# Kernel tuning notes

Measured on AMD Instinct MI355X. Metric: run time of the kernel, lower is better.

Reference implementation:

```python
import jax, jax.numpy as jnp
import numpy as np

D_MODEL = 512
NUM_HEADS = 8
DEPTH = D_MODEL // NUM_HEADS
BATCH = 16
SEQ = 1024


def setup_inputs() -> dict:
    key = jax.random.key(0)
    kq, kk, kv, k1, k2, k3, k4 = jax.random.split(key, 7)
    scale = 1.0 / np.sqrt(D_MODEL)
    return {
        "v": jax.random.normal(kv, (BATCH, SEQ, D_MODEL), jnp.float32),
        "k": jax.random.normal(kk, (BATCH, SEQ, D_MODEL), jnp.float32),
        "q": jax.random.normal(kq, (BATCH, SEQ, D_MODEL), jnp.float32),
        "mask": jnp.ones((BATCH, SEQ), jnp.float32),
        # Conv1D(kernel_size=1, use_bias=False) == per-token Linear: x @ W, W [d_in, d_out]
        "Wq": jax.random.normal(k1, (D_MODEL, D_MODEL), jnp.float32) * scale,
        "Wk": jax.random.normal(k2, (D_MODEL, D_MODEL), jnp.float32) * scale,
        "Wv": jax.random.normal(k3, (D_MODEL, D_MODEL), jnp.float32) * scale,
        "Wo": jax.random.normal(k4, (D_MODEL, D_MODEL), jnp.float32) * scale,
    }


def _split_heads(x, batch):
    # [b, s, d_model] -> [b, h, s, depth]
    return x.reshape(batch, -1, NUM_HEADS, DEPTH).transpose(0, 2, 1, 3)


def reference(v, k, q, mask, Wq, Wk, Wv, Wo):
    batch = q.shape[0]
    qh = _split_heads(q @ Wq, batch)  # [b,h,sq,dh]
    kh = _split_heads(k @ Wk, batch)  # [b,h,sk,dh]
    vh = _split_heads(v @ Wv, batch)  # [b,h,sk,dh]

    dk = jnp.asarray(DEPTH, qh.dtype)
    logits = jnp.einsum("bhqd,bhkd->bhqk", qh, kh) / jnp.sqrt(dk)
    # additive padding mask, broadcast [b,1,1,sk]
    logits = logits + (1.0 - mask[:, None, None, :]) * (-1e9)
    attention_weights = jax.nn.softmax(logits, axis=-1)  # [b,h,sq,sk]

    ctx = jnp.einsum("bhqk,bhkd->bhqd", attention_weights, vh)
    ctx = ctx.transpose(0, 2, 1, 3).reshape(batch, -1, D_MODEL)
    output = ctx @ Wo
    return output, attention_weights
```

## Files before the change

kernel.cpp:

```cpp
#include <hip/hip_runtime.h>


typedef _Float16 f16;
typedef _Float16 f16x8 __attribute__((ext_vector_type(8)));
typedef _Float16 f16x4 __attribute__((ext_vector_type(4)));
typedef float f32x4 __attribute__((ext_vector_type(4)));

#define DEVINL __device__ __forceinline__

static constexpr int BATCH = 16, SEQ = 1024, DM = 512, NH = 8, DH = 64;

DEVINL void async16(void* lds, const void* g) {
  __builtin_amdgcn_global_load_lds(
      (const __attribute__((address_space(1))) unsigned int*)g,
      (__attribute__((address_space(3))) unsigned int*)lds, 16, 0, 0);
}

__global__ __launch_bounds__(256) void prep_wt_k(
    const float* __restrict__ Wq, const float* __restrict__ Wk,
    const float* __restrict__ Wv, const float* __restrict__ Wo,
    f16* __restrict__ WT) {
  __shared__ float t[32][33];
  const int w = blockIdx.z;
  const float* src = (w == 0) ? Wq : (w == 1) ? Wk : (w == 2) ? Wv : Wo;
  const int k0 = blockIdx.y * 32, n0 = blockIdx.x * 32;
  const int r0 = threadIdx.x >> 5, c = threadIdx.x & 31;
#pragma unroll
  for (int i = 0; i < 4; ++i)
    t[i * 8 + r0][c] = src[(size_t)(k0 + i * 8 + r0) * DM + n0 + c];
  __syncthreads();
  f16* dst = WT + (size_t)w * DM * DM;
#pragma unroll
  for (int i = 0; i < 4; ++i)
    dst[(size_t)(n0 + i * 8 + r0) * DM + k0 + c] = (f16)t[c][i * 8 + r0];
}

template <int MODE>
DEVINL void gemm_body(const float* __restrict__ A32, const f16* __restrict__ A16,
                      const f16* __restrict__ WTn, f16* __restrict__ O16,
                      float* __restrict__ O32, int m0, int n0, bool vt) {
  __shared__ __align__(16) f16 As[2][128 * 32];
  __shared__ __align__(16) f16 Bs[2][128 * 32];
  const int tid = threadIdx.x;
  const int lane = tid & 63, wave = tid >> 6;
  const int wr = wave >> 1, wc = wave & 1;
  const int lrow = lane & 15, lkg = lane >> 4;
  f32x4 acc[4][4] = {};

  f32x4 ar[4];

  auto stageB = [&](int kt, int buf) {
#pragma unroll
    for (int it = 0; it < 2; ++it) {
      const int o = (it * 256 + tid) * 16;
      const int n = o >> 6, kb = o & 63;
      async16((char*)&Bs[buf][0] + (it * 256 + wave * 64) * 16,
              (const char*)WTn + ((size_t)(n0 + n) * DM + kt * 32) * 2 + kb);
    }
  };
  auto stageA_async = [&](int kt, int buf) {
#pragma unroll
    for (int it = 0; it < 2; ++it) {
      const int o = (it * 256 + tid) * 16;
      const int row = o >> 6, kb = o & 63;
      async16((char*)&As[buf][0] + (it * 256 + wave * 64) * 16,
              (const char*)A16 + ((size_t)(m0 + row) * DM + kt * 32) * 2 + kb);
    }
  };
  auto loadA = [&](int kt) {
#pragma unroll
    for (int c = 0; c < 4; ++c) {
      const int idx = c * 256 + tid;
      const int row = idx >> 3, sub = idx & 7;
      ar[c] = *(const f32x4*)(A32 + (size_t)(m0 + row) * DM + kt * 32 + sub * 4);
    }
  };
  auto writeA = [&](int buf) {
#pragma unroll
    for (int c = 0; c < 4; ++c) {
      const int idx = c * 256 + tid;
      const int row = idx >> 3, sub = idx & 7;
      f16x4 t;
      t[0] = (f16)ar[c][0]; t[1] = (f16)ar[c][1];
      t[2] = (f16)ar[c][2]; t[3] = (f16)ar[c][3];
      *(f16x4*)&As[buf][row * 32 + sub * 4] = t;
    }
  };

  stageB(0, 0);
  if (MODE == 0) {
    loadA(0);
    writeA(0);
  } else {
    stageA_async(0, 0);
  }
  __syncthreads();

  for (int kt = 0; kt < DM / 32; ++kt) {
    const int cur = kt & 1;
    if (kt < DM / 32 - 1) {
      stageB(kt + 1, cur ^ 1);
      if (MODE == 0) loadA(kt + 1);
      else stageA_async(kt + 1, cur ^ 1);
    }
    f16x8 af[4], bf[4];
#pragma unroll
    for (int i = 0; i < 4; ++i)
      af[i] = *(const f16x8*)&As[cur][(wr * 64 + i * 16 + lrow) * 32 + lkg * 8];
#pragma unroll
    for (int j = 0; j < 4; ++j)
      bf[j] = *(const f16x8*)&Bs[cur][(wc * 64 + j * 16 + lrow) * 32 + lkg * 8];
#pragma unroll
    for (int i = 0; i < 4; ++i)
#pragma unroll
      for (int j = 0; j < 4; ++j)
        acc[i][j] = __builtin_amdgcn_mfma_f32_16x16x32_f16(af[i], bf[j], acc[i][j], 0, 0, 0);
    if (MODE == 0 && kt < DM / 32 - 1) writeA(cur ^ 1);
    __syncthreads();
  }

#pragma unroll
  for (int i = 0; i < 4; ++i) {
#pragma unroll
    for (int j = 0; j < 4; ++j) {
#pragma unroll
      for (int r = 0; r < 4; ++r) {
        const int m = m0 + wr * 64 + i * 16 + lkg * 4 + r;
        const int g = n0 + wc * 64 + j * 16 + lrow;
        if (MODE == 0) {
          const int b = m >> 10, s = m & 1023, hh = g >> 6, d = g & 63;
          if (vt)
            O16[(((size_t)b * NH + hh) * DH + d) * SEQ + s] = (f16)acc[i][j][r];
          else
            O16[(((size_t)b * NH + hh) * SEQ + s) * DH + d] = (f16)acc[i][j][r];
        } else {
          O32[(size_t)m * DM + g] = acc[i][j][r];
        }
      }
    }
  }
}

__global__ __launch_bounds__(256, 2) void proj_k(
    const float* __restrict__ q, const float* __restrict__ k, const float* __restrict__ v,
    const f16* __restrict__ WT, f16* __restrict__ Qh, f16* __restrict__ Kh,
    f16* __restrict__ Vh) {
  const int bid = blockIdx.x;
  const int wid = (bid & 7) * 192 + (bid >> 3);
  const int n_blk = wid & 3, m_blk = (wid >> 2) & 127, z = wid >> 9;
  const float* A = (z == 0) ? q : (z == 1) ? k : v;
  const f16* W = WT + (size_t)z * DM * DM;
  f16* O = (z == 0) ? Qh : (z == 1) ? Kh : Vh;
  gemm_body<0>(A, nullptr, W, O, nullptr, m_blk * 128, n_blk * 128, z == 2);
}

__global__ __launch_bounds__(256, 2) void outp_k(const f16* __restrict__ ctx,
                                                 const f16* __restrict__ WoT,
                                                 float* __restrict__ out0) {
  const int bid = blockIdx.x;
  const int wid = (bid & 7) * 64 + (bid >> 3);
  const int n_blk = wid & 3, m_blk = wid >> 2;
  gemm_body<1>(nullptr, ctx, WoT, nullptr, out0, m_blk * 128, n_blk * 128, false);
}

__global__ __launch_bounds__(256, 3) void attn_k(
    const f16* __restrict__ Qh, const f16* __restrict__ Kh, const f16* __restrict__ VTh,
    const float* __restrict__ mask, float* __restrict__ attnW, f16* __restrict__ ctx) {
  __shared__ __align__(16) f16 Ks[2][64 * 64];
  __shared__ __align__(16) f16 Vt[2][64 * 64];
  __shared__ __align__(16) f16 Ps[4][16 * 64];
  __shared__ __align__(16) float Ms[SEQ];
  const int tid = threadIdx.x;
  const int lane = tid & 63, wave = tid >> 6;
  const int lq = lane & 15, g = lane >> 4;
  const int bid = blockIdx.x;
  const int wid = (bid & 7) * 256 + (bid >> 3);
  const int qt = wid & 15, h = (wid >> 4) & 7, b = wid >> 7;
  const size_t bh = (size_t)b * NH + h;
  const char* Kbase = (const char*)(Kh + bh * SEQ * DH);
  const char* VTbase = (const char*)(VTh + bh * (size_t)DH * SEQ);
  const int q0 = qt * 64 + wave * 16;

  auto stageK = [&](int kt, int buf) {
    const char* KtileB = Kbase + (size_t)kt * 64 * DH * 2;
#pragma unroll
    for (int it = 0; it < 2; ++it) {
      const int o = (it * 256 + tid) * 16;
      const int key = o >> 7, slot = (o >> 4) & 7;
      async16((char*)&Ks[buf][0] + (it * 256 + wave * 64) * 16,
              KtileB + key * 128 + ((slot ^ (key & 7)) << 4));
    }
  };
  auto stageV = [&](int kt, int buf) {
    const char* VtileB = VTbase + (size_t)kt * 64 * 2;
#pragma unroll
    for (int it = 0; it < 2; ++it) {
      const int o = (it * 256 + tid) * 16;
      const int d = o >> 7, slot = (o >> 4) & 7;
      async16((char*)&Vt[buf][0] + (it * 256 + wave * 64) * 16,
              VtileB + (size_t)d * (SEQ * 2) + ((slot ^ (d & 7)) << 4));
    }
  };

  {
    f32x4 mv = *(const f32x4*)(mask + (size_t)b * SEQ + tid * 4);
    f32x4 bv;
    bv[0] = (1.0f - mv[0]) * (-1e9f);
    bv[1] = (1.0f - mv[1]) * (-1e9f);
    bv[2] = (1.0f - mv[2]) * (-1e9f);
    bv[3] = (1.0f - mv[3]) * (-1e9f);
    *(f32x4*)&Ms[tid * 4] = bv;
  }

  f16x8 aQ0, aQ1;
  {
    const f16* qp = Qh + (bh * SEQ + q0 + lq) * DH + g * 8;
    aQ0 = *(const f16x8*)qp;
    aQ1 = *(const f16x8*)(qp + 32);
  }

  stageK(0, 0);
  __syncthreads();
  float ssum = 0.0f;
  for (int kt = 0; kt < 16; ++kt) {
    const int cur = kt & 1;
    if (kt < 15) stageK(kt + 1, cur ^ 1);
    f32x4 lg[4] = {};
#pragma unroll
    for (int j = 0; j < 4; ++j) {
      const int krow = j * 16 + lq;
      f16x8 a0 = *(const f16x8*)((const char*)&Ks[cur][0] + krow * 128 + ((g ^ (krow & 7)) << 4));
      f16x8 a1 = *(const f16x8*)((const char*)&Ks[cur][0] + krow * 128 + (((4 + g) ^ (krow & 7)) << 4));
      lg[j] = __builtin_amdgcn_mfma_f32_16x16x32_f16(a0, aQ0, lg[j], 0, 0, 0);
      lg[j] = __builtin_amdgcn_mfma_f32_16x16x32_f16(a1, aQ1, lg[j], 0, 0, 0);
    }
#pragma unroll
    for (int j = 0; j < 4; ++j) {
      f32x4 bias = *(const f32x4*)&Ms[kt * 64 + j * 16 + g * 4];
#pragma unroll
      for (int r = 0; r < 4; ++r) ssum += __expf(lg[j][r] * 0.125f + bias[r]);
    }
    __syncthreads();
  }

  ssum += __shfl_xor(ssum, 16);
  ssum += __shfl_xor(ssum, 32);
  const float inv = 1.0f / ssum;

  f32x4 ctxacc[4] = {};
  float* awBase = attnW + (bh * SEQ + q0) * SEQ;

  stageK(0, 0);
  stageV(0, 0);
  __syncthreads();
  for (int kt = 0; kt < 16; ++kt) {
    const int cur = kt & 1;
    if (kt < 15) {
      stageK(kt + 1, cur ^ 1);
      stageV(kt + 1, cur ^ 1);
    }
    f32x4 lg[4] = {};
#pragma unroll
    for (int j = 0; j < 4; ++j) {
      const int krow = j * 16 + lq;
      f16x8 a0 = *(const f16x8*)((const char*)&Ks[cur][0] + krow * 128 + ((g ^ (krow & 7)) << 4));
      f16x8 a1 = *(const f16x8*)((const char*)&Ks[cur][0] + krow * 128 + (((4 + g) ^ (krow & 7)) << 4));
      lg[j] = __builtin_amdgcn_mfma_f32_16x16x32_f16(a0, aQ0, lg[j], 0, 0, 0);
      lg[j] = __builtin_amdgcn_mfma_f32_16x16x32_f16(a1, aQ1, lg[j], 0, 0, 0);
    }
#pragma unroll
    for (int j = 0; j < 4; ++j) {
      f32x4 bias = *(const f32x4*)&Ms[kt * 64 + j * 16 + g * 4];
      f32x4 w;
#pragma unroll
      for (int r = 0; r < 4; ++r) w[r] = __expf(lg[j][r] * 0.125f + bias[r]) * inv;
      *(f32x4*)(awBase + (size_t)lq * SEQ + kt * 64 + j * 16 + g * 4) = w;
      f16x4 pw;
      pw[0] = (f16)w[0]; pw[1] = (f16)w[1]; pw[2] = (f16)w[2]; pw[3] = (f16)w[3];
      const int slot = 2 * j + (g >> 1);
      *(f16x4*)((char*)&Ps[wave][0] + lq * 128 + ((slot ^ (lq & 7)) << 4) + 8 * (g & 1)) = pw;
    }
#pragma unroll
    for (int kk = 0; kk < 2; ++kk) {
      f16x8 aP = *(const f16x8*)((const char*)&Ps[wave][0] + lq * 128 +
                                 (((4 * kk + g) ^ (lq & 7)) << 4));
#pragma unroll
      for (int j2 = 0; j2 < 4; ++j2) {
        const int drow = j2 * 16 + lq;
        f16x8 bV = *(const f16x8*)((const char*)&Vt[cur][0] + drow * 128 +
                                   (((4 * kk + g) ^ (drow & 7)) << 4));
        ctxacc[j2] = __builtin_amdgcn_mfma_f32_16x16x32_f16(aP, bV, ctxacc[j2], 0, 0, 0);
      }
    }
    __syncthreads();
  }

#pragma unroll
  for (int j2 = 0; j2 < 4; ++j2)
#pragma unroll
    for (int r = 0; r < 4; ++r) {
      const int s = q0 + g * 4 + r;
      const int d = j2 * 16 + lq;
      ctx[(((size_t)b * SEQ + s) * NH + h) * DH + d] = (f16)ctxacc[j2][r];
    }
}

extern "C" void kernel_launch(void* const* d_in, const int* in_sizes, int n_in,
                              void* d_out, int out_size, void* d_ws, size_t ws_size,
                              hipStream_t stream) {
  const float* v = (const float*)d_in[0];
  const float* k = (const float*)d_in[1];
  const float* q = (const float*)d_in[2];
  const float* mask = (const float*)d_in[3];
  const float* Wq = (const float*)d_in[4];
  const float* Wk = (const float*)d_in[5];
  const float* Wv = (const float*)d_in[6];
  const float* Wo = (const float*)d_in[7];

  float* out0 = (float*)d_out;
  float* attnW = out0 + (size_t)BATCH * SEQ * DM;

  char* ws = (char*)d_ws;
  f16* WT = (f16*)ws;
  f16* Qh = (f16*)(ws + (size_t)4 * DM * DM * 2);
  f16* Kh = Qh + (size_t)BATCH * NH * SEQ * DH;
  f16* VTh = Kh + (size_t)BATCH * NH * SEQ * DH;
  f16* ctx = VTh + (size_t)BATCH * NH * SEQ * DH;

  prep_wt_k<<<dim3(16, 16, 4), 256, 0, stream>>>(Wq, Wk, Wv, Wo, WT);
  proj_k<<<dim3(1536), 256, 0, stream>>>(q, k, v, WT, Qh, Kh, VTh);
  attn_k<<<dim3(2048), 256, 0, stream>>>(Qh, Kh, VTh, mask, attnW, ctx);
  outp_k<<<dim3(512), 256, 0, stream>>>(ctx, WT + (size_t)3 * DM * DM, out0);
}
```

Measured before the change: 341.9 us.

## Cache unnormalized probabilities in LDS to skip recomputing QK^T in second pass

The first pass now writes fp16 exp(logits) for the wave's full 16x1024 row block into a large LDS buffer. The second pass reads them back instead of restaging K and redoing the QK^T MFMAs and exponentials. The softmax normalization is applied when writing attention weights, and once to the context accumulator at the end. This removes the duplicate K loads and score computation. In exchange, LDS use grows to roughly 150KB per block, which limits occupancy to one block per CU, and the stored attention weights now come from fp16-rounded exponentials.

```diff
diff --git a/kernel.cpp b/kernel.cpp
--- a/kernel.cpp
+++ b/kernel.cpp
@@ -163,12 +163,11 @@
   gemm_body<1>(nullptr, ctx, WoT, nullptr, out0, m_blk * 128, n_blk * 128, false);
 }
 
-__global__ __launch_bounds__(256, 3) void attn_k(
+__global__ __launch_bounds__(256, 1) void attn_k(
     const f16* __restrict__ Qh, const f16* __restrict__ Kh, const f16* __restrict__ VTh,
     const float* __restrict__ mask, float* __restrict__ attnW, f16* __restrict__ ctx) {
-  __shared__ __align__(16) f16 Ks[2][64 * 64];
-  __shared__ __align__(16) f16 Vt[2][64 * 64];
-  __shared__ __align__(16) f16 Ps[4][16 * 64];
+  __shared__ __align__(16) f16 st[2][64 * 64];
+  __shared__ __align__(16) f16 Pw[4][16 * 1024];
   __shared__ __align__(16) float Ms[SEQ];
   const int tid = threadIdx.x;
   const int lane = tid & 63, wave = tid >> 6;
@@ -187,7 +186,7 @@
     for (int it = 0; it < 2; ++it) {
       const int o = (it * 256 + tid) * 16;
       const int key = o >> 7, slot = (o >> 4) & 7;
-      async16((char*)&Ks[buf][0] + (it * 256 + wave * 64) * 16,
+      async16((char*)&st[buf][0] + (it * 256 + wave * 64) * 16,
               KtileB + key * 128 + ((slot ^ (key & 7)) << 4));
     }
   };
@@ -197,7 +196,7 @@
     for (int it = 0; it < 2; ++it) {
       const int o = (it * 256 + tid) * 16;
       const int d = o >> 7, slot = (o >> 4) & 7;
-      async16((char*)&Vt[buf][0] + (it * 256 + wave * 64) * 16,
+      async16((char*)&st[buf][0] + (it * 256 + wave * 64) * 16,
               VtileB + (size_t)d * (SEQ * 2) + ((slot ^ (d & 7)) << 4));
     }
   };
@@ -229,16 +228,23 @@
 #pragma unroll
     for (int j = 0; j < 4; ++j) {
       const int krow = j * 16 + lq;
-      f16x8 a0 = *(const f16x8*)((const char*)&Ks[cur][0] + krow * 128 + ((g ^ (krow & 7)) << 4));
-      f16x8 a1 = *(const f16x8*)((const char*)&Ks[cur][0] + krow * 128 + (((4 + g) ^ (krow & 7)) << 4));
+      f16x8 a0 = *(const f16x8*)((const char*)&st[cur][0] + krow * 128 + ((g ^ (krow & 7)) << 4));
+      f16x8 a1 = *(const f16x8*)((const char*)&st[cur][0] + krow * 128 + (((4 + g) ^ (krow & 7)) << 4));
       lg[j] = __builtin_amdgcn_mfma_f32_16x16x32_f16(a0, aQ0, lg[j], 0, 0, 0);
       lg[j] = __builtin_amdgcn_mfma_f32_16x16x32_f16(a1, aQ1, lg[j], 0, 0, 0);
     }
 #pragma unroll
     for (int j = 0; j < 4; ++j) {
       f32x4 bias = *(const f32x4*)&Ms[kt * 64 + j * 16 + g * 4];
-#pragma unroll
-      for (int r = 0; r < 4; ++r) ssum += __expf(lg[j][r] * 0.125f + bias[r]);
+      f16x4 pw;
+#pragma unroll
+      for (int r = 0; r < 4; ++r) {
+        const float p = __expf(lg[j][r] * 0.125f + bias[r]);
+        pw[r] = (f16)p;
+        ssum += (float)pw[r];
+      }
+      const int s = kt * 8 + j * 2 + (g >> 1);
+      *(f16x4*)((char*)&Pw[wave][0] + lq * 2048 + ((s ^ (lq & 7)) << 4) + (g & 1) * 8) = pw;
     }
     __syncthreads();
   }
@@ -250,44 +256,29 @@
   f32x4 ctxacc[4] = {};
   float* awBase = attnW + (bh * SEQ + q0) * SEQ;
 
-  stageK(0, 0);
   stageV(0, 0);
   __syncthreads();
   for (int kt = 0; kt < 16; ++kt) {
     const int cur = kt & 1;
-    if (kt < 15) {
-      stageK(kt + 1, cur ^ 1);
-      stageV(kt + 1, cur ^ 1);
-    }
-    f32x4 lg[4] = {};
+    if (kt < 15) stageV(kt + 1, cur ^ 1);
 #pragma unroll
     for (int j = 0; j < 4; ++j) {
-      const int krow = j * 16 + lq;
-      f16x8 a0 = *(const f16x8*)((const char*)&Ks[cur][0] + krow * 128 + ((g ^ (krow & 7)) << 4));
-      f16x8 a1 = *(const f16x8*)((const char*)&Ks[cur][0] + krow * 128 + (((4 + g) ^ (krow & 7)) << 4));
-      lg[j] = __builtin_amdgcn_mfma_f32_16x16x32_f16(a0, aQ0, lg[j], 0, 0, 0);
-      lg[j] = __builtin_amdgcn_mfma_f32_16x16x32_f16(a1, aQ1, lg[j], 0, 0, 0);
-    }
-#pragma unroll
-    for (int j = 0; j < 4; ++j) {
-      f32x4 bias = *(const f32x4*)&Ms[kt * 64 + j * 16 + g * 4];
+      const int s = kt * 8 + j * 2 + (g >> 1);
+      f16x4 pw = *(const f16x4*)((const char*)&Pw[wave][0] + lq * 2048 +
+                                 ((s ^ (lq & 7)) << 4) + (g & 1) * 8);
       f32x4 w;
-#pragma unroll
-      for (int r = 0; r < 4; ++r) w[r] = __expf(lg[j][r] * 0.125f + bias[r]) * inv;
+      w[0] = (float)pw[0] * inv; w[1] = (float)pw[1] * inv;
+      w[2] = (float)pw[2] * inv; w[3] = (float)pw[3] * inv;
       *(f32x4*)(awBase + (size_t)lq * SEQ + kt * 64 + j * 16 + g * 4) = w;
-      f16x4 pw;
-      pw[0] = (f16)w[0]; pw[1] = (f16)w[1]; pw[2] = (f16)w[2]; pw[3] = (f16)w[3];
-      const int slot = 2 * j + (g >> 1);
-      *(f16x4*)((char*)&Ps[wave][0] + lq * 128 + ((slot ^ (lq & 7)) << 4) + 8 * (g & 1)) = pw;
     }
 #pragma unroll
     for (int kk = 0; kk < 2; ++kk) {
-      f16x8 aP = *(const f16x8*)((const char*)&Ps[wave][0] + lq * 128 +
-                                 (((4 * kk + g) ^ (lq & 7)) << 4));
+      const int s = kt * 8 + kk * 4 + g;
+      f16x8 aP = *(const f16x8*)((const char*)&Pw[wave][0] + lq * 2048 + ((s ^ (lq & 7)) << 4));
 #pragma unroll
       for (int j2 = 0; j2 < 4; ++j2) {
         const int drow = j2 * 16 + lq;
-        f16x8 bV = *(const f16x8*)((const char*)&Vt[cur][0] + drow * 128 +
+        f16x8 bV = *(const f16x8*)((const char*)&st[cur][0] + drow * 128 +
                                    (((4 * kk + g) ^ (drow & 7)) << 4));
         ctxacc[j2] = __builtin_amdgcn_mfma_f32_16x16x32_f16(aP, bV, ctxacc[j2], 0, 0, 0);
       }
@@ -295,13 +286,17 @@
     __syncthreads();
   }
 
+  float invR[4];
+#pragma unroll
+  for (int r = 0; r < 4; ++r) invR[r] = __shfl(inv, g * 4 + r, 64);
+
 #pragma unroll
   for (int j2 = 0; j2 < 4; ++j2)
 #pragma unroll
     for (int r = 0; r < 4; ++r) {
       const int s = q0 + g * 4 + r;
       const int d = j2 * 16 + lq;
-      ctx[(((size_t)b * SEQ + s) * NH + h) * DH + d] = (f16)ctxacc[j2][r];
+      ctx[(((size_t)b * SEQ + s) * NH + h) * DH + d] = (f16)(ctxacc[j2][r] * invR[r]);
     }
 }
 
```

New measurement: 457.4 us. 33.8% more time.

## Process four query subtiles per attention block to reuse staged K/V tiles

Applied to the files above, without the earlier changes.

Each attention block now handles 256 queries (four 16-row subtiles per wave) instead of 64, so every K and V tile staged in LDS feeds four times as many MFMAs. The grid shrinks from 2048 to 512 blocks and the launch bound drops to 2 waves-per-EU to make room for the larger accumulator and register footprint. This is meant to cut redundant global K/V reads and LDS staging. The cost is higher register pressure, a larger Ps buffer in LDS, and fewer blocks to hide latency on the attention-weight stores.

```diff
diff --git a/kernel.cpp b/kernel.cpp
--- a/kernel.cpp
+++ b/kernel.cpp
@@ -163,23 +163,23 @@
   gemm_body<1>(nullptr, ctx, WoT, nullptr, out0, m_blk * 128, n_blk * 128, false);
 }
 
-__global__ __launch_bounds__(256, 3) void attn_k(
+__global__ __launch_bounds__(256, 2) void attn_k(
     const f16* __restrict__ Qh, const f16* __restrict__ Kh, const f16* __restrict__ VTh,
     const float* __restrict__ mask, float* __restrict__ attnW, f16* __restrict__ ctx) {
   __shared__ __align__(16) f16 Ks[2][64 * 64];
   __shared__ __align__(16) f16 Vt[2][64 * 64];
-  __shared__ __align__(16) f16 Ps[4][16 * 64];
+  __shared__ __align__(16) f16 Ps[4][4][16 * 64];
   __shared__ __align__(16) float Ms[SEQ];
   const int tid = threadIdx.x;
   const int lane = tid & 63, wave = tid >> 6;
   const int lq = lane & 15, g = lane >> 4;
   const int bid = blockIdx.x;
-  const int wid = (bid & 7) * 256 + (bid >> 3);
-  const int qt = wid & 15, h = (wid >> 4) & 7, b = wid >> 7;
+  const int wid = (bid & 7) * 64 + (bid >> 3);
+  const int qt4 = wid & 3, h = (wid >> 2) & 7, b = wid >> 5;
   const size_t bh = (size_t)b * NH + h;
   const char* Kbase = (const char*)(Kh + bh * SEQ * DH);
   const char* VTbase = (const char*)(VTh + bh * (size_t)DH * SEQ);
-  const int q0 = qt * 64 + wave * 16;
+  const int qbase = qt4 * 256 + wave * 16;
 
   auto stageK = [&](int kt, int buf) {
     const char* KtileB = Kbase + (size_t)kt * 64 * DH * 2;
@@ -212,43 +212,55 @@
     *(f32x4*)&Ms[tid * 4] = bv;
   }
 
-  f16x8 aQ0, aQ1;
-  {
-    const f16* qp = Qh + (bh * SEQ + q0 + lq) * DH + g * 8;
-    aQ0 = *(const f16x8*)qp;
-    aQ1 = *(const f16x8*)(qp + 32);
-  }
-
+  f16x8 aQ0[4], aQ1[4];
+#pragma unroll
+  for (int st = 0; st < 4; ++st) {
+    const f16* qp = Qh + (bh * SEQ + qbase + st * 64 + lq) * DH + g * 8;
+    aQ0[st] = *(const f16x8*)qp;
+    aQ1[st] = *(const f16x8*)(qp + 32);
+  }
+
+  float ssum[4] = {0.f, 0.f, 0.f, 0.f};
   stageK(0, 0);
   __syncthreads();
-  float ssum = 0.0f;
   for (int kt = 0; kt < 16; ++kt) {
     const int cur = kt & 1;
     if (kt < 15) stageK(kt + 1, cur ^ 1);
-    f32x4 lg[4] = {};
+    f16x8 a0[4], a1[4];
 #pragma unroll
     for (int j = 0; j < 4; ++j) {
       const int krow = j * 16 + lq;
-      f16x8 a0 = *(const f16x8*)((const char*)&Ks[cur][0] + krow * 128 + ((g ^ (krow & 7)) << 4));
-      f16x8 a1 = *(const f16x8*)((const char*)&Ks[cur][0] + krow * 128 + (((4 + g) ^ (krow & 7)) << 4));
-      lg[j] = __builtin_amdgcn_mfma_f32_16x16x32_f16(a0, aQ0, lg[j], 0, 0, 0);
-      lg[j] = __builtin_amdgcn_mfma_f32_16x16x32_f16(a1, aQ1, lg[j], 0, 0, 0);
-    }
-#pragma unroll
-    for (int j = 0; j < 4; ++j) {
-      f32x4 bias = *(const f32x4*)&Ms[kt * 64 + j * 16 + g * 4];
-#pragma unroll
-      for (int r = 0; r < 4; ++r) ssum += __expf(lg[j][r] * 0.125f + bias[r]);
+      a0[j] = *(const f16x8*)((const char*)&Ks[cur][0] + krow * 128 + ((g ^ (krow & 7)) << 4));
+      a1[j] = *(const f16x8*)((const char*)&Ks[cur][0] + krow * 128 + (((4 + g) ^ (krow & 7)) << 4));
+    }
+#pragma unroll
+    for (int st = 0; st < 4; ++st) {
+      f32x4 lg[4] = {};
+#pragma unroll
+      for (int j = 0; j < 4; ++j) {
+        lg[j] = __builtin_amdgcn_mfma_f32_16x16x32_f16(a0[j], aQ0[st], lg[j], 0, 0, 0);
+        lg[j] = __builtin_amdgcn_mfma_f32_16x16x32_f16(a1[j], aQ1[st], lg[j], 0, 0, 0);
+      }
+#pragma unroll
+      for (int j = 0; j < 4; ++j) {
+        f32x4 bias = *(const f32x4*)&Ms[kt * 64 + j * 16 + g * 4];
+#pragma unroll
+        for (int r = 0; r < 4; ++r) ssum[st] += __expf(lg[j][r] * 0.125f + bias[r]);
+      }
     }
     __syncthreads();
   }
 
-  ssum += __shfl_xor(ssum, 16);
-  ssum += __shfl_xor(ssum, 32);
-  const float inv = 1.0f / ssum;
-
-  f32x4 ctxacc[4] = {};
-  float* awBase = attnW + (bh * SEQ + q0) * SEQ;
+  float inv[4];
+#pragma unroll
+  for (int st = 0; st < 4; ++st) {
+    float s = ssum[st];
+    s += __shfl_xor(s, 16);
+    s += __shfl_xor(s, 32);
+    inv[st] = 1.0f / s;
+  }
+
+  f32x4 ctxacc[4][4] = {};
 
   stageK(0, 0);
   stageV(0, 0);
@@ -259,50 +271,68 @@
       stageK(kt + 1, cur ^ 1);
       stageV(kt + 1, cur ^ 1);
     }
-    f32x4 lg[4] = {};
+    f16x8 a0[4], a1[4];
 #pragma unroll
     for (int j = 0; j < 4; ++j) {
       const int krow = j * 16 + lq;
-      f16x8 a0 = *(const f16x8*)((const char*)&Ks[cur][0] + krow * 128 + ((g ^ (krow & 7)) << 4));
-      f16x8 a1 = *(const f16x8*)((const char*)&Ks[cur][0] + krow * 128 + (((4 + g) ^ (krow & 7)) << 4));
-      lg[j] = __builtin_amdgcn_mfma_f32_16x16x32_f16(a0, aQ0, lg[j], 0, 0, 0);
-      lg[j] = __builtin_amdgcn_mfma_f32_16x16x32_f16(a1, aQ1, lg[j], 0, 0, 0);
-    }
-#pragma unroll
-    for (int j = 0; j < 4; ++j) {
-      f32x4 bias = *(const f32x4*)&Ms[kt * 64 + j * 16 + g * 4];
-      f32x4 w;
-#pragma unroll
-      for (int r = 0; r < 4; ++r) w[r] = __expf(lg[j][r] * 0.125f + bias[r]) * inv;
-      *(f32x4*)(awBase + (size_t)lq * SEQ + kt * 64 + j * 16 + g * 4) = w;
-      f16x4 pw;
-      pw[0] = (f16)w[0]; pw[1] = (f16)w[1]; pw[2] = (f16)w[2]; pw[3] = (f16)w[3];
-      const int slot = 2 * j + (g >> 1);
-      *(f16x4*)((char*)&Ps[wave][0] + lq * 128 + ((slot ^ (lq & 7)) << 4) + 8 * (g & 1)) = pw;
+      a0[j] = *(const f16x8*)((const char*)&Ks[cur][0] + krow * 128 + ((g ^ (krow & 7)) << 4));
+      a1[j] = *(const f16x8*)((const char*)&Ks[cur][0] + krow * 128 + (((4 + g) ^ (krow & 7)) << 4));
+    }
+#pragma unroll
+    for (int st = 0; st < 4; ++st) {
+      f32x4 lg[4] = {};
+#pragma unroll
+      for (int j = 0; j < 4; ++j) {
+        lg[j] = __builtin_amdgcn_mfma_f32_16x16x32_f16(a0[j], aQ0[st], lg[j], 0, 0, 0);
+        lg[j] = __builtin_amdgcn_mfma_f32_16x16x32_f16(a1[j], aQ1[st], lg[j], 0, 0, 0);
+      }
+      float* awRow = attnW + ((bh * SEQ + qbase + st * 64 + lq) * SEQ) + kt * 64 + g * 4;
+      char* psBase = (char*)&Ps[wave][st][0] + lq * 128;
+#pragma unroll
+      for (int j = 0; j < 4; ++j) {
+        f32x4 bias = *(const f32x4*)&Ms[kt * 64 + j * 16 + g * 4];
+        f32x4 w;
+#pragma unroll
+        for (int r = 0; r < 4; ++r) w[r] = __expf(lg[j][r] * 0.125f + bias[r]) * inv[st];
+        *(f32x4*)(awRow + j * 16) = w;
+        f16x4 pw;
+        pw[0] = (f16)w[0]; pw[1] = (f16)w[1]; pw[2] = (f16)w[2]; pw[3] = (f16)w[3];
+        const int slot = 2 * j + (g >> 1);
+        *(f16x4*)(psBase + ((slot ^ (lq & 7)) << 4) + (g & 1) * 8) = pw;
+      }
     }
 #pragma unroll
     for (int kk = 0; kk < 2; ++kk) {
-      f16x8 aP = *(const f16x8*)((const char*)&Ps[wave][0] + lq * 128 +
-                                 (((4 * kk + g) ^ (lq & 7)) << 4));
+      f16x8 aP[4];
+#pragma unroll
+      for (int st = 0; st < 4; ++st) {
+        const int s = 4 * kk + g;
+        aP[st] = *(const f16x8*)((const char*)&Ps[wave][st][0] + lq * 128 +
+                                 ((s ^ (lq & 7)) << 4));
+      }
 #pragma unroll
       for (int j2 = 0; j2 < 4; ++j2) {
         const int drow = j2 * 16 + lq;
         f16x8 bV = *(const f16x8*)((const char*)&Vt[cur][0] + drow * 128 +
                                    (((4 * kk + g) ^ (drow & 7)) << 4));
-        ctxacc[j2] = __builtin_amdgcn_mfma_f32_16x16x32_f16(aP, bV, ctxacc[j2], 0, 0, 0);
+#pragma unroll
+        for (int st = 0; st < 4; ++st)
+          ctxacc[st][j2] = __builtin_amdgcn_mfma_f32_16x16x32_f16(aP[st], bV, ctxacc[st][j2], 0, 0, 0);
       }
     }
     __syncthreads();
   }
 
 #pragma unroll
-  for (int j2 = 0; j2 < 4; ++j2)
-#pragma unroll
-    for (int r = 0; r < 4; ++r) {
-      const int s = q0 + g * 4 + r;
-      const int d = j2 * 16 + lq;
-      ctx[(((size_t)b * SEQ + s) * NH + h) * DH + d] = (f16)ctxacc[j2][r];
-    }
+  for (int st = 0; st < 4; ++st)
+#pragma unroll
+    for (int j2 = 0; j2 < 4; ++j2)
+#pragma unroll
+      for (int r = 0; r < 4; ++r) {
+        const int s = qbase + st * 64 + g * 4 + r;
+        const int d = j2 * 16 + lq;
+        ctx[(((size_t)b * SEQ + s) * NH + h) * DH + d] = (f16)ctxacc[st][j2][r];
+      }
 }
 
 extern "C" void kernel_launch(void* const* d_in, const int* in_sizes, int n_in,
@@ -329,6 +359,6 @@
 
   prep_wt_k<<<dim3(16, 16, 4), 256, 0, stream>>>(Wq, Wk, Wv, Wo, WT);
   proj_k<<<dim3(1536), 256, 0, stream>>>(q, k, v, WT, Qh, Kh, VTh);
-  attn_k<<<dim3(2048), 256, 0, stream>>>(Qh, Kh, VTh, mask, attnW, ctx);
+  attn_k<<<dim3(512), 256, 0, stream>>>(Qh, Kh, VTh, mask, attnW, ctx);
   outp_k<<<dim3(512), 256, 0, stream>>>(ctx, WT + (size_t)3 * DM * DM, out0);
 }
```

Result: faster. 327.8 us (-4.1%).
